# Kernel tuning notes

Measured on AMD Instinct MI355X. Metric: run time of the kernel, lower is better.

Reference implementation:

```python
import jax, jax.numpy as jnp
import numpy as np


def setup_inputs() -> dict:
    key = jax.random.key(0)
    k1, k2, k3 = jax.random.split(key, 3)
    B, S, D = 128, 1024, 64
    return {
        "q": jax.random.normal(k1, (B, S, D), dtype=jnp.float32),
        "k": jax.random.normal(k2, (B, S, D), dtype=jnp.float32),
        "v": jax.random.normal(k3, (B, S, D), dtype=jnp.float32),
    }


def reference(q, k, v):
    # Faithful to the torch module: NO 1/sqrt(d) scaling.
    # Chunking over batch dim in the original is math-equivalent to full bmm.
    scores = jnp.einsum("bsd,btd->bst", q, k)  # [B, S, S]
    attn = jax.nn.softmax(scores, axis=-1)
    return jnp.einsum("bst,btd->bsd", attn, v)  # [B, S, D]
```

## Files before the change

kernel.cpp:

```cpp
#include <hip/hip_runtime.h>
#include <math.h>

namespace {

typedef _Float16 half8 __attribute__((ext_vector_type(8)));
typedef float floatx4 __attribute__((ext_vector_type(4)));

constexpr int kS   = 1024;
constexpr int kD   = 64;
constexpr int kPad = 72;
constexpr float kLog2e = 1.4426950408889634f;
constexpr float kThr   = 8.0f;

union H4 { _Float16 h[4]; uint2 u2; };

__device__ __forceinline__ float fast_exp2(float x) {
#if __has_builtin(__builtin_amdgcn_exp2f)
  return __builtin_amdgcn_exp2f(x);
#else
  return exp2f(x);
#endif
}

__device__ __forceinline__ float fast_rcp(float x) {
#if __has_builtin(__builtin_amdgcn_rcpf)
  return __builtin_amdgcn_rcpf(x);
#else
  return 1.0f / x;
#endif
}

__global__ __launch_bounds__(256, 3)
void fa_mfma_kernel(const float* __restrict__ qg, const float* __restrict__ kg,
                    const float* __restrict__ vg, float* __restrict__ og) {
  __shared__ __align__(16) _Float16 sK [64][kPad];
  __shared__ __align__(16) _Float16 sVt[64][kPad];
  __shared__ __align__(16) _Float16 sP [128][kPad];

  const int tid  = threadIdx.x;
  const int lane = tid & 63;
  const int w    = __builtin_amdgcn_readfirstlane(tid >> 6);
  const int quad = lane >> 4;
  const int r    = lane & 15;

  const int blk = blockIdx.x;
  const int s   = blk >> 3;
  const int b   = (blk & 7) + 8 * (s & 15);
  const int qbase = (s >> 4) * 128;

  const float* qb = qg + (size_t)b * kS * kD;
  const float* kb = kg + (size_t)b * kS * kD;
  const float* vb = vg + (size_t)b * kS * kD;
  float*       ob = og + (size_t)b * kS * kD;

  half8 fqh[2][2], fql[2][2];
#pragma unroll
  for (int ntq = 0; ntq < 2; ++ntq)
#pragma unroll
    for (int ks = 0; ks < 2; ++ks) {
      const float* src =
          qb + (size_t)(qbase + w * 32 + ntq * 16 + r) * kD + ks * 32 + quad * 8;
      float4 a = ((const float4*)src)[0];
      float4 c = ((const float4*)src)[1];
      float f[8] = {a.x, a.y, a.z, a.w, c.x, c.y, c.z, c.w};
#pragma unroll
      for (int j = 0; j < 8; ++j) {
        float x = f[j] * kLog2e;
        _Float16 h = (_Float16)x;
        fqh[ntq][ks][j] = h;
        fql[ntq][ks][j] = (_Float16)(x - (float)h);
      }
    }

  float m_i[2] = {-INFINITY, -INFINITY}, l_i[2] = {0.f, 0.f};
  floatx4 O[2][4];
#pragma unroll
  for (int a = 0; a < 2; ++a)
#pragma unroll
    for (int c = 0; c < 4; ++c) O[a][c] = floatx4{0.f, 0.f, 0.f, 0.f};

  const int krow = tid >> 2, kc0 = (tid & 3) * 16;
  const int vkey4 = (tid & 15) * 4;
  const int vd0   = (tid >> 4) * 4;
  float4 kbuf[4], vbuf[4];
  {
    const float4* ksrc = (const float4*)(kb + (size_t)krow * kD + kc0);
#pragma unroll
    for (int g = 0; g < 4; ++g) kbuf[g] = ksrc[g];
#pragma unroll
    for (int kk = 0; kk < 4; ++kk)
      vbuf[kk] = *(const float4*)(vb + (size_t)(vkey4 + kk) * kD + vd0);
  }

  for (int kt = 0; kt < kS / 64; ++kt) {
    __syncthreads();
#pragma unroll
    for (int g = 0; g < 4; ++g) {
      float t[4] = {kbuf[g].x, kbuf[g].y, kbuf[g].z, kbuf[g].w};
      H4 hk;
#pragma unroll
      for (int j = 0; j < 4; ++j) hk.h[j] = (_Float16)t[j];
      *(uint2*)&sK[krow][kc0 + g * 4] = hk.u2;
    }
    {
      float tv[4][4];
#pragma unroll
      for (int kk = 0; kk < 4; ++kk) {
        tv[kk][0] = vbuf[kk].x; tv[kk][1] = vbuf[kk].y;
        tv[kk][2] = vbuf[kk].z; tv[kk][3] = vbuf[kk].w;
      }
#pragma unroll
      for (int j = 0; j < 4; ++j) {
        H4 hv;
#pragma unroll
        for (int kk = 0; kk < 4; ++kk) hv.h[kk] = (_Float16)tv[kk][j];
        *(uint2*)&sVt[vd0 + j][vkey4] = hv.u2;
      }
    }
    {
      const int ktn = (kt + 1) & 15;
      const float4* ksrc =
          (const float4*)(kb + (size_t)(ktn * 64 + krow) * kD + kc0);
#pragma unroll
      for (int g = 0; g < 4; ++g) kbuf[g] = ksrc[g];
#pragma unroll
      for (int kk = 0; kk < 4; ++kk)
        vbuf[kk] =
            *(const float4*)(vb + (size_t)(ktn * 64 + vkey4 + kk) * kD + vd0);
    }
    __syncthreads();

    floatx4 S[2][4];
    __builtin_amdgcn_s_setprio(1);
#pragma unroll
    for (int mt = 0; mt < 4; ++mt) {
      half8 fk0 = *(const half8*)&sK[mt * 16 + r][0 * 32 + quad * 8];
      half8 fk1 = *(const half8*)&sK[mt * 16 + r][1 * 32 + quad * 8];
#pragma unroll
      for (int ntq = 0; ntq < 2; ++ntq) {
        floatx4 ah = {0.f, 0.f, 0.f, 0.f}, al = {0.f, 0.f, 0.f, 0.f};
        ah = __builtin_amdgcn_mfma_f32_16x16x32_f16(fk0, fqh[ntq][0], ah, 0, 0, 0);
        ah = __builtin_amdgcn_mfma_f32_16x16x32_f16(fk1, fqh[ntq][1], ah, 0, 0, 0);
        al = __builtin_amdgcn_mfma_f32_16x16x32_f16(fk0, fql[ntq][0], al, 0, 0, 0);
        al = __builtin_amdgcn_mfma_f32_16x16x32_f16(fk1, fql[ntq][1], al, 0, 0, 0);
        S[ntq][mt] = ah + al;
      }
    }
    __builtin_amdgcn_s_setprio(0);

    float tm[2];
#pragma unroll
    for (int ntq = 0; ntq < 2; ++ntq) {
      float t = -INFINITY;
#pragma unroll
      for (int mt = 0; mt < 4; ++mt)
#pragma unroll
        for (int j = 0; j < 4; ++j) t = fmaxf(t, S[ntq][mt][j]);
      t = fmaxf(t, __shfl_xor(t, 16, 64));
      t = fmaxf(t, __shfl_xor(t, 32, 64));
      tm[ntq] = t;
    }
    const unsigned long long need =
        __ballot(tm[0] > m_i[0] + kThr || tm[1] > m_i[1] + kThr);
    if (need) {
      float alpha[2];
#pragma unroll
      for (int ntq = 0; ntq < 2; ++ntq) {
        const float mn = fmaxf(m_i[ntq], tm[ntq]);
        alpha[ntq] = fast_exp2(m_i[ntq] - mn);
        m_i[ntq] = mn;
        l_i[ntq] *= alpha[ntq];
      }
#pragma unroll
      for (int mtq = 0; mtq < 2; ++mtq)
#pragma unroll
        for (int j = 0; j < 4; ++j) {
          const float a = __shfl(alpha[mtq], quad * 4 + j, 64);
#pragma unroll
          for (int nd = 0; nd < 4; ++nd) O[mtq][nd][j] *= a;
        }
    }
#pragma unroll
    for (int ntq = 0; ntq < 2; ++ntq) {
      float rs = 0.f;
#pragma unroll
      for (int mt = 0; mt < 4; ++mt) {
        H4 hp;
#pragma unroll
        for (int j = 0; j < 4; ++j) {
          float pj = fast_exp2(S[ntq][mt][j] - m_i[ntq]);
          rs += pj;
          hp.h[j] = (_Float16)pj;
        }
        *(uint2*)&sP[w * 32 + ntq * 16 + r][mt * 16 + quad * 4] = hp.u2;
      }
      rs += __shfl_xor(rs, 16, 64);
      rs += __shfl_xor(rs, 32, 64);
      l_i[ntq] += rs;
    }

    __builtin_amdgcn_s_setprio(1);
#pragma unroll
    for (int ks = 0; ks < 2; ++ks) {
      half8 fp0 = *(const half8*)&sP[w * 32 + 0 * 16 + r][ks * 32 + quad * 8];
      half8 fp1 = *(const half8*)&sP[w * 32 + 1 * 16 + r][ks * 32 + quad * 8];
#pragma unroll
      for (int nd = 0; nd < 4; ++nd) {
        half8 fv = *(const half8*)&sVt[nd * 16 + r][ks * 32 + quad * 8];
        O[0][nd] = __builtin_amdgcn_mfma_f32_16x16x32_f16(fp0, fv, O[0][nd], 0, 0, 0);
        O[1][nd] = __builtin_amdgcn_mfma_f32_16x16x32_f16(fp1, fv, O[1][nd], 0, 0, 0);
      }
    }
    __builtin_amdgcn_s_setprio(0);
  }

#pragma unroll
  for (int mtq = 0; mtq < 2; ++mtq)
#pragma unroll
    for (int j = 0; j < 4; ++j) {
      const float lrow = __shfl(l_i[mtq], quad * 4 + j, 64);
      const float linv = fast_rcp(lrow);
      float* dst =
          ob + (size_t)(qbase + w * 32 + mtq * 16 + quad * 4 + j) * kD + r;
#pragma unroll
      for (int nd = 0; nd < 4; ++nd) dst[nd * 16] = O[mtq][nd][j] * linv;
    }
}

}

extern "C" void kernel_launch(void* const* d_in, const int* in_sizes, int n_in,
                              void* d_out, int out_size, void* d_ws, size_t ws_size,
                              hipStream_t stream) {
  const float* q = (const float*)d_in[0];
  const float* k = (const float*)d_in[1];
  const float* v = (const float*)d_in[2];
  float* out = (float*)d_out;

  fa_mfma_kernel<<<dim3(1024), 256, 0, stream>>>(q, k, v, out);
}
```

Before: 195.2 us.

## Double query rows per block to reuse K/V tiles across more queries

Each block now processes 256 query rows (64 per wave) instead of 128, halving the grid to 512 blocks and lowering the occupancy hint to 2 blocks per CU. K/V tiles loaded and converted into shared memory are reused by twice as many queries, cutting global K/V traffic and conversion work. The score/softmax stage is split into two halves to limit live registers. It risks higher register pressure and less latency hiding from fewer resident waves.

```diff
diff --git a/kernel.cpp b/kernel.cpp
--- a/kernel.cpp
+++ b/kernel.cpp
@@ -30,12 +30,12 @@
 #endif
 }
 
-__global__ __launch_bounds__(256, 3)
+__global__ __launch_bounds__(256, 2)
 void fa_mfma_kernel(const float* __restrict__ qg, const float* __restrict__ kg,
                     const float* __restrict__ vg, float* __restrict__ og) {
   __shared__ __align__(16) _Float16 sK [64][kPad];
   __shared__ __align__(16) _Float16 sVt[64][kPad];
-  __shared__ __align__(16) _Float16 sP [128][kPad];
+  __shared__ __align__(16) _Float16 sP [256][kPad];
 
   const int tid  = threadIdx.x;
   const int lane = tid & 63;
@@ -44,22 +44,21 @@
   const int r    = lane & 15;
 
   const int blk = blockIdx.x;
-  const int s   = blk >> 3;
-  const int b   = (blk & 7) + 8 * (s & 15);
-  const int qbase = (s >> 4) * 128;
+  const int b     = (blk & 7) + 8 * (blk >> 5);
+  const int qbase = ((blk >> 3) & 3) * 256;
 
   const float* qb = qg + (size_t)b * kS * kD;
   const float* kb = kg + (size_t)b * kS * kD;
   const float* vb = vg + (size_t)b * kS * kD;
   float*       ob = og + (size_t)b * kS * kD;
 
-  half8 fqh[2][2], fql[2][2];
-#pragma unroll
-  for (int ntq = 0; ntq < 2; ++ntq)
+  half8 fqh[4][2], fql[4][2];
+#pragma unroll
+  for (int ntq = 0; ntq < 4; ++ntq)
 #pragma unroll
     for (int ks = 0; ks < 2; ++ks) {
       const float* src =
-          qb + (size_t)(qbase + w * 32 + ntq * 16 + r) * kD + ks * 32 + quad * 8;
+          qb + (size_t)(qbase + w * 64 + ntq * 16 + r) * kD + ks * 32 + quad * 8;
       float4 a = ((const float4*)src)[0];
       float4 c = ((const float4*)src)[1];
       float f[8] = {a.x, a.y, a.z, a.w, c.x, c.y, c.z, c.w};
@@ -72,10 +71,11 @@
       }
     }
 
-  float m_i[2] = {-INFINITY, -INFINITY}, l_i[2] = {0.f, 0.f};
-  floatx4 O[2][4];
-#pragma unroll
-  for (int a = 0; a < 2; ++a)
+  float m_i[4] = {-INFINITY, -INFINITY, -INFINITY, -INFINITY};
+  float l_i[4] = {0.f, 0.f, 0.f, 0.f};
+  floatx4 O[4][4];
+#pragma unroll
+  for (int a = 0; a < 4; ++a)
 #pragma unroll
     for (int c = 0; c < 4; ++c) O[a][c] = floatx4{0.f, 0.f, 0.f, 0.f};
 
@@ -130,98 +130,110 @@
     }
     __syncthreads();
 
-    floatx4 S[2][4];
+#pragma unroll
+    for (int h = 0; h < 2; ++h) {
+      floatx4 S[2][4];
+      __builtin_amdgcn_s_setprio(1);
+#pragma unroll
+      for (int mt = 0; mt < 4; ++mt) {
+        half8 fk0 = *(const half8*)&sK[mt * 16 + r][0 * 32 + quad * 8];
+        half8 fk1 = *(const half8*)&sK[mt * 16 + r][1 * 32 + quad * 8];
+#pragma unroll
+        for (int g = 0; g < 2; ++g) {
+          const int ntq = h * 2 + g;
+          floatx4 ah = {0.f, 0.f, 0.f, 0.f}, al = {0.f, 0.f, 0.f, 0.f};
+          ah = __builtin_amdgcn_mfma_f32_16x16x32_f16(fk0, fqh[ntq][0], ah, 0, 0, 0);
+          ah = __builtin_amdgcn_mfma_f32_16x16x32_f16(fk1, fqh[ntq][1], ah, 0, 0, 0);
+          al = __builtin_amdgcn_mfma_f32_16x16x32_f16(fk0, fql[ntq][0], al, 0, 0, 0);
+          al = __builtin_amdgcn_mfma_f32_16x16x32_f16(fk1, fql[ntq][1], al, 0, 0, 0);
+          S[g][mt] = ah + al;
+        }
+      }
+      __builtin_amdgcn_s_setprio(0);
+
+      float tm[2];
+#pragma unroll
+      for (int g = 0; g < 2; ++g) {
+        float t = -INFINITY;
+#pragma unroll
+        for (int mt = 0; mt < 4; ++mt)
+#pragma unroll
+          for (int j = 0; j < 4; ++j) t = fmaxf(t, S[g][mt][j]);
+        t = fmaxf(t, __shfl_xor(t, 16, 64));
+        t = fmaxf(t, __shfl_xor(t, 32, 64));
+        tm[g] = t;
+      }
+      const unsigned long long need =
+          __ballot(tm[0] > m_i[h * 2] + kThr || tm[1] > m_i[h * 2 + 1] + kThr);
+      if (need) {
+        float alpha[2];
+#pragma unroll
+        for (int g = 0; g < 2; ++g) {
+          const int ntq = h * 2 + g;
+          const float mn = fmaxf(m_i[ntq], tm[g]);
+          alpha[g] = fast_exp2(m_i[ntq] - mn);
+          m_i[ntq] = mn;
+          l_i[ntq] *= alpha[g];
+        }
+#pragma unroll
+        for (int g = 0; g < 2; ++g) {
+          const int mtq = h * 2 + g;
+#pragma unroll
+          for (int j = 0; j < 4; ++j) {
+            const float a = __shfl(alpha[g], quad * 4 + j, 64);
+#pragma unroll
+            for (int nd = 0; nd < 4; ++nd) O[mtq][nd][j] *= a;
+          }
+        }
+      }
+#pragma unroll
+      for (int g = 0; g < 2; ++g) {
+        const int ntq = h * 2 + g;
+        float rs = 0.f;
+#pragma unroll
+        for (int mt = 0; mt < 4; ++mt) {
+          H4 hp;
+#pragma unroll
+          for (int j = 0; j < 4; ++j) {
+            float pj = fast_exp2(S[g][mt][j] - m_i[ntq]);
+            rs += pj;
+            hp.h[j] = (_Float16)pj;
+          }
+          *(uint2*)&sP[w * 64 + ntq * 16 + r][mt * 16 + quad * 4] = hp.u2;
+        }
+        rs += __shfl_xor(rs, 16, 64);
+        rs += __shfl_xor(rs, 32, 64);
+        l_i[ntq] += rs;
+      }
+    }
+
     __builtin_amdgcn_s_setprio(1);
 #pragma unroll
-    for (int mt = 0; mt < 4; ++mt) {
-      half8 fk0 = *(const half8*)&sK[mt * 16 + r][0 * 32 + quad * 8];
-      half8 fk1 = *(const half8*)&sK[mt * 16 + r][1 * 32 + quad * 8];
-#pragma unroll
-      for (int ntq = 0; ntq < 2; ++ntq) {
-        floatx4 ah = {0.f, 0.f, 0.f, 0.f}, al = {0.f, 0.f, 0.f, 0.f};
-        ah = __builtin_amdgcn_mfma_f32_16x16x32_f16(fk0, fqh[ntq][0], ah, 0, 0, 0);
-        ah = __builtin_amdgcn_mfma_f32_16x16x32_f16(fk1, fqh[ntq][1], ah, 0, 0, 0);
-        al = __builtin_amdgcn_mfma_f32_16x16x32_f16(fk0, fql[ntq][0], al, 0, 0, 0);
-        al = __builtin_amdgcn_mfma_f32_16x16x32_f16(fk1, fql[ntq][1], al, 0, 0, 0);
-        S[ntq][mt] = ah + al;
-      }
-    }
-    __builtin_amdgcn_s_setprio(0);
-
-    float tm[2];
-#pragma unroll
-    for (int ntq = 0; ntq < 2; ++ntq) {
-      float t = -INFINITY;
-#pragma unroll
-      for (int mt = 0; mt < 4; ++mt)
-#pragma unroll
-        for (int j = 0; j < 4; ++j) t = fmaxf(t, S[ntq][mt][j]);
-      t = fmaxf(t, __shfl_xor(t, 16, 64));
-      t = fmaxf(t, __shfl_xor(t, 32, 64));
-      tm[ntq] = t;
-    }
-    const unsigned long long need =
-        __ballot(tm[0] > m_i[0] + kThr || tm[1] > m_i[1] + kThr);
-    if (need) {
-      float alpha[2];
-#pragma unroll
-      for (int ntq = 0; ntq < 2; ++ntq) {
-        const float mn = fmaxf(m_i[ntq], tm[ntq]);
-        alpha[ntq] = fast_exp2(m_i[ntq] - mn);
-        m_i[ntq] = mn;
-        l_i[ntq] *= alpha[ntq];
-      }
-#pragma unroll
-      for (int mtq = 0; mtq < 2; ++mtq)
-#pragma unroll
-        for (int j = 0; j < 4; ++j) {
-          const float a = __shfl(alpha[mtq], quad * 4 + j, 64);
-#pragma unroll
-          for (int nd = 0; nd < 4; ++nd) O[mtq][nd][j] *= a;
-        }
-    }
-#pragma unroll
-    for (int ntq = 0; ntq < 2; ++ntq) {
-      float rs = 0.f;
-#pragma unroll
-      for (int mt = 0; mt < 4; ++mt) {
-        H4 hp;
-#pragma unroll
-        for (int j = 0; j < 4; ++j) {
-          float pj = fast_exp2(S[ntq][mt][j] - m_i[ntq]);
-          rs += pj;
-          hp.h[j] = (_Float16)pj;
-        }
-        *(uint2*)&sP[w * 32 + ntq * 16 + r][mt * 16 + quad * 4] = hp.u2;
-      }
-      rs += __shfl_xor(rs, 16, 64);
-      rs += __shfl_xor(rs, 32, 64);
-      l_i[ntq] += rs;
-    }
-
-    __builtin_amdgcn_s_setprio(1);
-#pragma unroll
     for (int ks = 0; ks < 2; ++ks) {
-      half8 fp0 = *(const half8*)&sP[w * 32 + 0 * 16 + r][ks * 32 + quad * 8];
-      half8 fp1 = *(const half8*)&sP[w * 32 + 1 * 16 + r][ks * 32 + quad * 8];
+      half8 fp[4];
+#pragma unroll
+      for (int mtq = 0; mtq < 4; ++mtq)
+        fp[mtq] = *(const half8*)&sP[w * 64 + mtq * 16 + r][ks * 32 + quad * 8];
 #pragma unroll
       for (int nd = 0; nd < 4; ++nd) {
         half8 fv = *(const half8*)&sVt[nd * 16 + r][ks * 32 + quad * 8];
-        O[0][nd] = __builtin_amdgcn_mfma_f32_16x16x32_f16(fp0, fv, O[0][nd], 0, 0, 0);
-        O[1][nd] = __builtin_amdgcn_mfma_f32_16x16x32_f16(fp1, fv, O[1][nd], 0, 0, 0);
+#pragma unroll
+        for (int mtq = 0; mtq < 4; ++mtq)
+          O[mtq][nd] =
+              __builtin_amdgcn_mfma_f32_16x16x32_f16(fp[mtq], fv, O[mtq][nd], 0, 0, 0);
       }
     }
     __builtin_amdgcn_s_setprio(0);
   }
 
 #pragma unroll
-  for (int mtq = 0; mtq < 2; ++mtq)
+  for (int mtq = 0; mtq < 4; ++mtq)
 #pragma unroll
     for (int j = 0; j < 4; ++j) {
       const float lrow = __shfl(l_i[mtq], quad * 4 + j, 64);
       const float linv = fast_rcp(lrow);
       float* dst =
-          ob + (size_t)(qbase + w * 32 + mtq * 16 + quad * 4 + j) * kD + r;
+          ob + (size_t)(qbase + w * 64 + mtq * 16 + quad * 4 + j) * kD + r;
 #pragma unroll
       for (int nd = 0; nd < 4; ++nd) dst[nd * 16] = O[mtq][nd][j] * linv;
     }
@@ -237,5 +249,5 @@
   const float* v = (const float*)d_in[2];
   float* out = (float*)d_out;
 
-  fa_mfma_kernel<<<dim3(1024), 256, 0, stream>>>(q, k, v, out);
-}
+  fa_mfma_kernel<<<dim3(512), 256, 0, stream>>>(q, k, v, out);
+}
```

After: 172.7 us. -11.5%, faster.

## Double-buffer K/V in LDS with 512-thread blocks and split K/V loader waves

Applied to the files above, without the earlier changes.

Grows each block to 8 waves covering 256 query rows, halving the grid so each K/V tile staged in LDS is reused by twice as many queries. K and V shared tiles are double-buffered, which drops one of the two barriers per iteration and stages the next tile while the current one is consumed. K and V global loads are split between two groups of waves to cut per-thread prefetch registers. The hi and lo score MFMAs also chain into a single accumulator instead of adding two. Risks are register pressure under the tighter launch bounds and fewer blocks for load balance.

```diff
diff --git a/kernel.cpp b/kernel.cpp
--- a/kernel.cpp
+++ b/kernel.cpp
@@ -30,12 +30,12 @@
 #endif
 }
 
-__global__ __launch_bounds__(256, 3)
+__global__ __launch_bounds__(512, 4)
 void fa_mfma_kernel(const float* __restrict__ qg, const float* __restrict__ kg,
                     const float* __restrict__ vg, float* __restrict__ og) {
-  __shared__ __align__(16) _Float16 sK [64][kPad];
-  __shared__ __align__(16) _Float16 sVt[64][kPad];
-  __shared__ __align__(16) _Float16 sP [128][kPad];
+  __shared__ __align__(16) _Float16 sK [2][64][kPad];
+  __shared__ __align__(16) _Float16 sVt[2][64][kPad];
+  __shared__ __align__(16) _Float16 sP [256][kPad];
 
   const int tid  = threadIdx.x;
   const int lane = tid & 63;
@@ -44,9 +44,8 @@
   const int r    = lane & 15;
 
   const int blk = blockIdx.x;
-  const int s   = blk >> 3;
-  const int b   = (blk & 7) + 8 * (s & 15);
-  const int qbase = (s >> 4) * 128;
+  const int b     = (blk & 7) + 8 * (blk >> 5);
+  const int qbase = ((blk >> 3) & 3) * 256;
 
   const float* qb = qg + (size_t)b * kS * kD;
   const float* kb = kg + (size_t)b * kS * kD;
@@ -79,124 +78,129 @@
 #pragma unroll
     for (int c = 0; c < 4; ++c) O[a][c] = floatx4{0.f, 0.f, 0.f, 0.f};
 
-  const int krow = tid >> 2, kc0 = (tid & 3) * 16;
-  const int vkey4 = (tid & 15) * 4;
-  const int vd0   = (tid >> 4) * 4;
-  float4 kbuf[4], vbuf[4];
-  {
-    const float4* ksrc = (const float4*)(kb + (size_t)krow * kD + kc0);
-#pragma unroll
-    for (int g = 0; g < 4; ++g) kbuf[g] = ksrc[g];
-#pragma unroll
-    for (int kk = 0; kk < 4; ++kk)
-      vbuf[kk] = *(const float4*)(vb + (size_t)(vkey4 + kk) * kD + vd0);
-  }
-
-  for (int kt = 0; kt < kS / 64; ++kt) {
-    __syncthreads();
-#pragma unroll
-    for (int g = 0; g < 4; ++g) {
-      float t[4] = {kbuf[g].x, kbuf[g].y, kbuf[g].z, kbuf[g].w};
-      H4 hk;
-#pragma unroll
-      for (int j = 0; j < 4; ++j) hk.h[j] = (_Float16)t[j];
-      *(uint2*)&sK[krow][kc0 + g * 4] = hk.u2;
-    }
-    {
+  const bool kRole = (w < 4);
+  const int st = tid & 255;
+  const int krow  = st >> 2, kc0 = (st & 3) * 16;
+  const int vkey4 = (st & 15) * 4;
+  const int vd0   = (st >> 4) * 4;
+  float4 buf[4];
+
+  auto load_kv = [&](int kt) {
+    if (kRole) {
+      const float4* ksrc =
+          (const float4*)(kb + (size_t)(kt * 64 + krow) * kD + kc0);
+#pragma unroll
+      for (int g = 0; g < 4; ++g) buf[g] = ksrc[g];
+    } else {
+#pragma unroll
+      for (int kk = 0; kk < 4; ++kk)
+        buf[kk] = *(const float4*)(vb + (size_t)(kt * 64 + vkey4 + kk) * kD + vd0);
+    }
+  };
+  auto stage = [&](int bi) {
+    if (kRole) {
+#pragma unroll
+      for (int g = 0; g < 4; ++g) {
+        float t[4] = {buf[g].x, buf[g].y, buf[g].z, buf[g].w};
+        H4 hk;
+#pragma unroll
+        for (int j = 0; j < 4; ++j) hk.h[j] = (_Float16)t[j];
+        *(uint2*)&sK[bi][krow][kc0 + g * 4] = hk.u2;
+      }
+    } else {
       float tv[4][4];
 #pragma unroll
       for (int kk = 0; kk < 4; ++kk) {
-        tv[kk][0] = vbuf[kk].x; tv[kk][1] = vbuf[kk].y;
-        tv[kk][2] = vbuf[kk].z; tv[kk][3] = vbuf[kk].w;
+        tv[kk][0] = buf[kk].x; tv[kk][1] = buf[kk].y;
+        tv[kk][2] = buf[kk].z; tv[kk][3] = buf[kk].w;
       }
 #pragma unroll
       for (int j = 0; j < 4; ++j) {
         H4 hv;
 #pragma unroll
         for (int kk = 0; kk < 4; ++kk) hv.h[kk] = (_Float16)tv[kk][j];
-        *(uint2*)&sVt[vd0 + j][vkey4] = hv.u2;
-      }
-    }
-    {
-      const int ktn = (kt + 1) & 15;
-      const float4* ksrc =
-          (const float4*)(kb + (size_t)(ktn * 64 + krow) * kD + kc0);
-#pragma unroll
-      for (int g = 0; g < 4; ++g) kbuf[g] = ksrc[g];
-#pragma unroll
-      for (int kk = 0; kk < 4; ++kk)
-        vbuf[kk] =
-            *(const float4*)(vb + (size_t)(ktn * 64 + vkey4 + kk) * kD + vd0);
-    }
+        *(uint2*)&sVt[bi][vd0 + j][vkey4] = hv.u2;
+      }
+    }
+  };
+
+  load_kv(0);
+  stage(0);
+  load_kv(1);
+
+  for (int kt = 0; kt < kS / 64; ++kt) {
+    const int cur = kt & 1, nxt = cur ^ 1;
     __syncthreads();
+    stage(nxt);
+    load_kv((kt + 2) & 15);
 
     floatx4 S[2][4];
     __builtin_amdgcn_s_setprio(1);
 #pragma unroll
     for (int mt = 0; mt < 4; ++mt) {
-      half8 fk0 = *(const half8*)&sK[mt * 16 + r][0 * 32 + quad * 8];
-      half8 fk1 = *(const half8*)&sK[mt * 16 + r][1 * 32 + quad * 8];
-#pragma unroll
-      for (int ntq = 0; ntq < 2; ++ntq) {
-        floatx4 ah = {0.f, 0.f, 0.f, 0.f}, al = {0.f, 0.f, 0.f, 0.f};
-        ah = __builtin_amdgcn_mfma_f32_16x16x32_f16(fk0, fqh[ntq][0], ah, 0, 0, 0);
-        ah = __builtin_amdgcn_mfma_f32_16x16x32_f16(fk1, fqh[ntq][1], ah, 0, 0, 0);
-        al = __builtin_amdgcn_mfma_f32_16x16x32_f16(fk0, fql[ntq][0], al, 0, 0, 0);
-        al = __builtin_amdgcn_mfma_f32_16x16x32_f16(fk1, fql[ntq][1], al, 0, 0, 0);
-        S[ntq][mt] = ah + al;
+      half8 fk0 = *(const half8*)&sK[cur][mt * 16 + r][quad * 8];
+      half8 fk1 = *(const half8*)&sK[cur][mt * 16 + r][32 + quad * 8];
+#pragma unroll
+      for (int g = 0; g < 2; ++g) {
+        floatx4 s = {0.f, 0.f, 0.f, 0.f};
+        s = __builtin_amdgcn_mfma_f32_16x16x32_f16(fk0, fqh[g][0], s, 0, 0, 0);
+        s = __builtin_amdgcn_mfma_f32_16x16x32_f16(fk1, fqh[g][1], s, 0, 0, 0);
+        s = __builtin_amdgcn_mfma_f32_16x16x32_f16(fk0, fql[g][0], s, 0, 0, 0);
+        s = __builtin_amdgcn_mfma_f32_16x16x32_f16(fk1, fql[g][1], s, 0, 0, 0);
+        S[g][mt] = s;
       }
     }
     __builtin_amdgcn_s_setprio(0);
 
     float tm[2];
 #pragma unroll
-    for (int ntq = 0; ntq < 2; ++ntq) {
+    for (int g = 0; g < 2; ++g) {
       float t = -INFINITY;
 #pragma unroll
       for (int mt = 0; mt < 4; ++mt)
 #pragma unroll
-        for (int j = 0; j < 4; ++j) t = fmaxf(t, S[ntq][mt][j]);
+        for (int j = 0; j < 4; ++j) t = fmaxf(t, S[g][mt][j]);
       t = fmaxf(t, __shfl_xor(t, 16, 64));
       t = fmaxf(t, __shfl_xor(t, 32, 64));
-      tm[ntq] = t;
+      tm[g] = t;
     }
     const unsigned long long need =
         __ballot(tm[0] > m_i[0] + kThr || tm[1] > m_i[1] + kThr);
     if (need) {
       float alpha[2];
 #pragma unroll
-      for (int ntq = 0; ntq < 2; ++ntq) {
-        const float mn = fmaxf(m_i[ntq], tm[ntq]);
-        alpha[ntq] = fast_exp2(m_i[ntq] - mn);
-        m_i[ntq] = mn;
-        l_i[ntq] *= alpha[ntq];
-      }
-#pragma unroll
-      for (int mtq = 0; mtq < 2; ++mtq)
+      for (int g = 0; g < 2; ++g) {
+        const float mn = fmaxf(m_i[g], tm[g]);
+        alpha[g] = fast_exp2(m_i[g] - mn);
+        m_i[g] = mn;
+        l_i[g] *= alpha[g];
+      }
+#pragma unroll
+      for (int g = 0; g < 2; ++g)
 #pragma unroll
         for (int j = 0; j < 4; ++j) {
-          const float a = __shfl(alpha[mtq], quad * 4 + j, 64);
-#pragma unroll
-          for (int nd = 0; nd < 4; ++nd) O[mtq][nd][j] *= a;
+          const float a = __shfl(alpha[g], quad * 4 + j, 64);
+#pragma unroll
+          for (int nd = 0; nd < 4; ++nd) O[g][nd][j] *= a;
         }
     }
 #pragma unroll
-    for (int ntq = 0; ntq < 2; ++ntq) {
+    for (int g = 0; g < 2; ++g) {
       float rs = 0.f;
 #pragma unroll
       for (int mt = 0; mt < 4; ++mt) {
         H4 hp;
 #pragma unroll
         for (int j = 0; j < 4; ++j) {
-          float pj = fast_exp2(S[ntq][mt][j] - m_i[ntq]);
+          float pj = fast_exp2(S[g][mt][j] - m_i[g]);
           rs += pj;
           hp.h[j] = (_Float16)pj;
         }
-        *(uint2*)&sP[w * 32 + ntq * 16 + r][mt * 16 + quad * 4] = hp.u2;
+        *(uint2*)&sP[w * 32 + g * 16 + r][mt * 16 + quad * 4] = hp.u2;
       }
       rs += __shfl_xor(rs, 16, 64);
       rs += __shfl_xor(rs, 32, 64);
-      l_i[ntq] += rs;
+      l_i[g] += rs;
     }
 
     __builtin_amdgcn_s_setprio(1);
@@ -206,7 +210,7 @@
       half8 fp1 = *(const half8*)&sP[w * 32 + 1 * 16 + r][ks * 32 + quad * 8];
 #pragma unroll
       for (int nd = 0; nd < 4; ++nd) {
-        half8 fv = *(const half8*)&sVt[nd * 16 + r][ks * 32 + quad * 8];
+        half8 fv = *(const half8*)&sVt[cur][nd * 16 + r][ks * 32 + quad * 8];
         O[0][nd] = __builtin_amdgcn_mfma_f32_16x16x32_f16(fp0, fv, O[0][nd], 0, 0, 0);
         O[1][nd] = __builtin_amdgcn_mfma_f32_16x16x32_f16(fp1, fv, O[1][nd], 0, 0, 0);
       }
@@ -237,5 +241,5 @@
   const float* v = (const float*)d_in[2];
   float* out = (float*)d_out;
 
-  fa_mfma_kernel<<<dim3(1024), 256, 0, stream>>>(q, k, v, out);
-}
+  fa_mfma_kernel<<<dim3(512), 512, 0, stream>>>(q, k, v, out);
+}
```

Result: slower. 277.2 us (+42.0%).
